# Performance work log

Hardware: AMD Instinct MI355X
Metric: run time of the kernel (lower is better)

## Reference

```python
import jax, jax.numpy as jnp
import numpy as np

N, E, F, H, ED, C, G = 50000, 800000, 86, 128, 16, 18, 64
NEG_SLOPE = 0.2


def setup_inputs() -> dict:
    key = jax.random.key(0)
    ks = jax.random.split(key, 20)
    s = 0.1
    return {
        "x": jax.random.normal(ks[0], (N, F), jnp.float32),
        "edge_index": jax.random.randint(ks[1], (2, E), 0, N, jnp.int32),
        "edge_attr": jax.random.normal(ks[2], (E, ED), jnp.float32),
        "batch": jnp.sort(jax.random.randint(ks[3], (N,), 0, G, jnp.int32)),
        # conv1 params (GATConv, heads=1): lin, lin_edge (no bias), att vectors, bias
        "W1": jax.random.normal(ks[4], (F, H), jnp.float32) * s,
        "We1": jax.random.normal(ks[5], (ED, H), jnp.float32) * s,
        "as1": jax.random.normal(ks[6], (H,), jnp.float32) * s,
        "ad1": jax.random.normal(ks[7], (H,), jnp.float32) * s,
        "ae1": jax.random.normal(ks[8], (H,), jnp.float32) * s,
        "b1": jnp.zeros((H,), jnp.float32),
        # conv2 params
        "W2": jax.random.normal(ks[9], (H, H), jnp.float32) * s,
        "We2": jax.random.normal(ks[10], (ED, H), jnp.float32) * s,
        "as2": jax.random.normal(ks[11], (H,), jnp.float32) * s,
        "ad2": jax.random.normal(ks[12], (H,), jnp.float32) * s,
        "ae2": jax.random.normal(ks[13], (H,), jnp.float32) * s,
        "b2": jnp.zeros((H,), jnp.float32),
        # final classifier
        "Wl": jax.random.normal(ks[14], (H, C), jnp.float32) * s,
        "bl": jnp.zeros((C,), jnp.float32),
    }


def gat_conv(x, edge_attr, src, dst, W, We, a_src, a_dst, a_edge, bias):
    h = x @ W                                   # [N, H]
    e = edge_attr @ We                          # [E, H]
    # per-edge attention logits: a_src.h_j + a_dst.h_i + a_edge.e
    alpha = (h @ a_src)[src] + (h @ a_dst)[dst] + e @ a_edge   # [E]
    alpha = jax.nn.leaky_relu(alpha, NEG_SLOPE)
    # segment softmax over incoming edges of each destination node
    m = jax.ops.segment_max(alpha, dst, num_segments=N)
    ex = jnp.exp(alpha - m[dst])
    denom = jax.ops.segment_sum(ex, dst, num_segments=N)
    w = ex / jnp.maximum(denom[dst], 1e-16)     # [E]
    out = jax.ops.segment_sum(h[src] * w[:, None], dst, num_segments=N)
    return out + bias


def reference(x, edge_index, edge_attr, batch,
              W1, We1, as1, ad1, ae1, b1,
              W2, We2, as2, ad2, ae2, b2,
              Wl, bl):
    src, dst = edge_index[0], edge_index[1]
    h = jax.nn.relu(gat_conv(x, edge_attr, src, dst, W1, We1, as1, ad1, ae1, b1))
    h = jax.nn.relu(gat_conv(h, edge_attr, src, dst, W2, We2, as2, ad2, ae2, b2))
    pooled = jax.ops.segment_max(h, batch, num_segments=G)      # [G, H] global max pool
    pooled = jnp.where(jnp.isfinite(pooled), pooled, 0.0)       # guard empty graphs
    logits = pooled @ Wl + bl                                   # [G, C]
    return jax.nn.log_softmax(logits, axis=-1)
```

## Files before the change

### kernel.cpp

```cpp
#include <hip/hip_runtime.h>
#include <math.h>

#define N_NODES 50000
#define N_EDGES 800000
#define F_IN    86
#define H_DIM   128
#define ED_DIM  16
#define C_CLS   18
#define G_GRAPHS 64
#define NEG_SLOPE 0.2f
#define SCAN_BLOCKS ((N_NODES + 255) / 256)
#define EB_BLOCKS ((N_EDGES + 255) / 256)
#define GB_BLOCKS ((N_NODES + 63) / 64)
#define HB_BLOCKS 782
#define HB_THREADS (HB_BLOCKS * 256)

typedef _Float16 h2v   __attribute__((ext_vector_type(2)));
typedef _Float16 half8 __attribute__((ext_vector_type(8)));
typedef float    f4v   __attribute__((ext_vector_type(4)));
typedef unsigned long long ull;

__device__ __forceinline__ void atomicMaxFloat(float* addr, float val) {
    if (val >= 0.0f) atomicMax((int*)addr, __float_as_int(val));
    else             atomicMin((unsigned int*)addr, __float_as_uint(val));
}

__global__ void prep(int* __restrict__ cnt0, int* __restrict__ cnt1,
                     float* __restrict__ pooled,
                     const float* __restrict__ We1, const float* __restrict__ ae1,
                     const float* __restrict__ We2, const float* __restrict__ ae2,
                     float* __restrict__ ve1, float* __restrict__ ve2,
                     const float* __restrict__ W1, const float* __restrict__ W2,
                     _Float16* __restrict__ w1t, _Float16* __restrict__ w2t) {
    int b = blockIdx.x, t = threadIdx.x;
    if (b < SCAN_BLOCKS) {
        int i = b * 256 + t;
        if (i < N_NODES) { cnt0[i] = 0; cnt1[i] = 0; }
    } else if (b == SCAN_BLOCKS) {
        if (t < ED_DIM) {
            float s = 0.f;
            for (int h = 0; h < H_DIM; ++h) s += We1[t * H_DIM + h] * ae1[h];
            ve1[t] = s;
        } else if (t < 2 * ED_DIM) {
            int j = t - ED_DIM;
            float s = 0.f;
            for (int h = 0; h < H_DIM; ++h) s += We2[j * H_DIM + h] * ae2[h];
            ve2[j] = s;
        }
        for (int i = t; i < G_GRAPHS * H_DIM; i += 256) pooled[i] = 0.f;
    } else if (b == SCAN_BLOCKS + 1) {
        for (int i = t; i < H_DIM * 96; i += 256) {
            int n = i / 96, k = i - n * 96;
            w1t[i] = (k < F_IN) ? (_Float16)W1[k * H_DIM + n] : (_Float16)0.f;
        }
    } else {
        for (int i = t; i < H_DIM * H_DIM; i += 256) {
            int n = i >> 7, k = i & 127;
            w2t[i] = (_Float16)W2[k * H_DIM + n];
        }
    }
}

__global__ void scan1(const int* __restrict__ cnt0, const int* __restrict__ cnt1,
                      int* __restrict__ excl, int* __restrict__ bsum) {
    __shared__ int s[256];
    int tid = threadIdx.x;
    int i = blockIdx.x * 256 + tid;
    int v = (i < N_NODES) ? cnt0[i] + cnt1[i] : 0;
    s[tid] = v;
    __syncthreads();
    for (int o = 1; o < 256; o <<= 1) {
        int t = (tid >= o) ? s[tid - o] : 0;
        __syncthreads();
        s[tid] += t;
        __syncthreads();
    }
    if (i < N_NODES) excl[i] = s[tid] - v;
    if (tid == 255) bsum[blockIdx.x] = s[255];
}

__global__ void scan_scatter(const int* __restrict__ excl, const int* __restrict__ bsum,
                             int* __restrict__ row_ptr,
                             const int* __restrict__ src, const int* __restrict__ dst,
                             const unsigned short* __restrict__ rank,
                             const int* __restrict__ cnt0,
                             const float* __restrict__ ea,
                             const float* __restrict__ ve1, const float* __restrict__ ve2,
                             int2* __restrict__ perm) {
    __shared__ int s[256];
    int tid = threadIdx.x;
    int v = (tid < SCAN_BLOCKS) ? bsum[tid] : 0;
    s[tid] = v;
    __syncthreads();
    for (int o = 1; o < 256; o <<= 1) {
        int t = (tid >= o) ? s[tid - o] : 0;
        __syncthreads();
        s[tid] += t;
        __syncthreads();
    }
    int eb = s[tid] - v;
    __syncthreads();
    s[tid] = eb;
    __syncthreads();
    int e = blockIdx.x * 256 + tid;
    if (blockIdx.x < SCAN_BLOCKS) {
        if (e < N_NODES) row_ptr[e] = excl[e] + s[e >> 8];
        if (e == 0) row_ptr[N_NODES] = N_EDGES;
    }
    if (e < N_EDGES) {
        int d = dst[e];
        int base = excl[d] + s[d >> 8];
        int off = (e & 1) ? cnt0[d] : 0;
        int pos = base + off + rank[e];
        const float4* p = (const float4*)(ea + (size_t)e * ED_DIM);
        float4 v0 = p[0], v1 = p[1], v2 = p[2], v3 = p[3];
        float s1 = v0.x*ve1[0] + v0.y*ve1[1] + v0.z*ve1[2] + v0.w*ve1[3]
                 + v1.x*ve1[4] + v1.y*ve1[5] + v1.z*ve1[6] + v1.w*ve1[7]
                 + v2.x*ve1[8] + v2.y*ve1[9] + v2.z*ve1[10] + v2.w*ve1[11]
                 + v3.x*ve1[12] + v3.y*ve1[13] + v3.z*ve1[14] + v3.w*ve1[15];
        float s2 = v0.x*ve2[0] + v0.y*ve2[1] + v0.z*ve2[2] + v0.w*ve2[3]
                 + v1.x*ve2[4] + v1.y*ve2[5] + v1.z*ve2[6] + v1.w*ve2[7]
                 + v2.x*ve2[8] + v2.y*ve2[9] + v2.z*ve2[10] + v2.w*ve2[11]
                 + v3.x*ve2[12] + v3.y*ve2[13] + v3.z*ve2[14] + v3.w*ve2[15];
        h2v dv;
        dv.x = (_Float16)s1;
        dv.y = (_Float16)s2;
        perm[pos] = make_int2(src[e], (int)__builtin_bit_cast(unsigned int, dv));
    }
}

#define KP1 104
__global__ __launch_bounds__(256)
void gemm1_hist(const float* __restrict__ in, const _Float16* __restrict__ w1t,
                const float* __restrict__ a_s, const float* __restrict__ a_d,
                _Float16* __restrict__ hout, float* __restrict__ hs, float* __restrict__ hd,
                const int* __restrict__ dst, int* __restrict__ cnt0, int* __restrict__ cnt1,
                unsigned short* __restrict__ rank) {
    __shared__ __attribute__((aligned(16))) _Float16 Asm[64 * KP1];
    __shared__ float sdots[64][2][2];
    int tid = threadIdx.x;

    if (blockIdx.x >= GB_BLOCKS) {
        int tbase = (blockIdx.x - GB_BLOCKS) * 256 + tid;
        int* bank = (tbase & 1) ? cnt1 : cnt0;
#pragma unroll
        for (int u = 0; u < 4; ++u) {
            int e = tbase + u * HB_THREADS;
            if (e < N_EDGES) {
                int r = atomicAdd(&bank[dst[e]], 1);
                rank[e] = (unsigned short)r;
            }
        }
        return;
    }

    int n0 = blockIdx.x * 64;
    const float2* in2 = (const float2*)(in + (size_t)n0 * F_IN);
    for (int idx = tid; idx < 64 * (F_IN / 2); idx += 256) {
        int r = idx / (F_IN / 2), k2 = idx - r * (F_IN / 2);
        float2 v = (n0 + r < N_NODES) ? in2[idx] : make_float2(0.f, 0.f);
        Asm[r * KP1 + 2 * k2]     = (_Float16)v.x;
        Asm[r * KP1 + 2 * k2 + 1] = (_Float16)v.y;
    }
    for (int idx = tid; idx < 64 * (96 - F_IN); idx += 256) {
        int r = idx / (96 - F_IN), k = F_IN + idx - r * (96 - F_IN);
        Asm[r * KP1 + k] = (_Float16)0.f;
    }
    __syncthreads();

    int wave = tid >> 6, lane = tid & 63;
    int wm = (wave & 1) * 32, wn = (wave >> 1) * 64;
    int m16 = lane & 15, quad = lane >> 4;

    f4v acc[2][4];
#pragma unroll
    for (int t = 0; t < 2; ++t)
#pragma unroll
        for (int c = 0; c < 4; ++c) acc[t][c] = (f4v){0.f, 0.f, 0.f, 0.f};

#pragma unroll
    for (int kk = 0; kk < 96 / 32; ++kk) {
        int koff = kk * 32 + quad * 8;
        half8 a0 = *(const half8*)&Asm[(wm + m16) * KP1 + koff];
        half8 a1 = *(const half8*)&Asm[(wm + 16 + m16) * KP1 + koff];
#pragma unroll
        for (int c = 0; c < 4; ++c) {
            half8 b = *(const half8*)&w1t[(wn + c * 16 + m16) * 96 + koff];
            acc[0][c] = __builtin_amdgcn_mfma_f32_16x16x32_f16(a0, b, acc[0][c], 0, 0, 0);
            acc[1][c] = __builtin_amdgcn_mfma_f32_16x16x32_f16(a1, b, acc[1][c], 0, 0, 0);
        }
    }

    float asv[4], adv[4];
#pragma unroll
    for (int c = 0; c < 4; ++c) {
        asv[c] = a_s[wn + c * 16 + m16];
        adv[c] = a_d[wn + c * 16 + m16];
    }
#pragma unroll
    for (int t = 0; t < 2; ++t)
#pragma unroll
        for (int r = 0; r < 4; ++r) {
            float ps = 0.f, pd = 0.f;
#pragma unroll
            for (int c = 0; c < 4; ++c) {
                float v = acc[t][c][r];
                ps += v * asv[c];
                pd += v * adv[c];
            }
#pragma unroll
            for (int o = 1; o < 16; o <<= 1) {
                ps += __shfl_xor(ps, o);
                pd += __shfl_xor(pd, o);
            }
            if (m16 == 0) {
                int row = wm + t * 16 + quad * 4 + r;
                sdots[row][wn >> 6][0] = ps;
                sdots[row][wn >> 6][1] = pd;
            }
        }
#pragma unroll
    for (int t = 0; t < 2; ++t)
#pragma unroll
        for (int c = 0; c < 4; ++c)
#pragma unroll
            for (int r = 0; r < 4; ++r) {
                int row = n0 + wm + t * 16 + quad * 4 + r;
                if (row < N_NODES)
                    hout[(size_t)row * H_DIM + wn + c * 16 + m16] = (_Float16)acc[t][c][r];
            }
    __syncthreads();
    if (tid < 64) {
        int row = n0 + tid;
        if (row < N_NODES) {
            hs[row] = sdots[tid][0][0] + sdots[tid][1][0];
            hd[row] = sdots[tid][0][1] + sdots[tid][1][1];
        }
    }
}

#define KP2 136
__global__ __launch_bounds__(256)
void gemm2(const _Float16* __restrict__ in, const _Float16* __restrict__ w2t,
           const float* __restrict__ a_s, const float* __restrict__ a_d,
           _Float16* __restrict__ hout, float* __restrict__ hs, float* __restrict__ hd) {
    __shared__ __attribute__((aligned(16))) _Float16 Asm[64 * KP2];
    __shared__ float sdots[64][2][2];
    int tid = threadIdx.x;
    int n0 = blockIdx.x * 64;

    const half8* in8 = (const half8*)(in + (size_t)n0 * H_DIM);
    for (int idx = tid; idx < 64 * 16; idx += 256) {
        int r = idx >> 4, k8 = idx & 15;
        half8 v = (n0 + r < N_NODES) ? in8[idx]
                                     : (half8){0, 0, 0, 0, 0, 0, 0, 0};
        *(half8*)&Asm[r * KP2 + k8 * 8] = v;
    }
    __syncthreads();

    int wave = tid >> 6, lane = tid & 63;
    int wm = (wave & 1) * 32, wn = (wave >> 1) * 64;
    int m16 = lane & 15, quad = lane >> 4;

    f4v acc[2][4];
#pragma unroll
    for (int t = 0; t < 2; ++t)
#pragma unroll
        for (int c = 0; c < 4; ++c) acc[t][c] = (f4v){0.f, 0.f, 0.f, 0.f};

#pragma unroll
    for (int kk = 0; kk < 128 / 32; ++kk) {
        int koff = kk * 32 + quad * 8;
        half8 a0 = *(const half8*)&Asm[(wm + m16) * KP2 + koff];
        half8 a1 = *(const half8*)&Asm[(wm + 16 + m16) * KP2 + koff];
#pragma unroll
        for (int c = 0; c < 4; ++c) {
            half8 b = *(const half8*)&w2t[(wn + c * 16 + m16) * H_DIM + koff];
            acc[0][c] = __builtin_amdgcn_mfma_f32_16x16x32_f16(a0, b, acc[0][c], 0, 0, 0);
            acc[1][c] = __builtin_amdgcn_mfma_f32_16x16x32_f16(a1, b, acc[1][c], 0, 0, 0);
        }
    }

    float asv[4], adv[4];
#pragma unroll
    for (int c = 0; c < 4; ++c) {
        asv[c] = a_s[wn + c * 16 + m16];
        adv[c] = a_d[wn + c * 16 + m16];
    }
#pragma unroll
    for (int t = 0; t < 2; ++t)
#pragma unroll
        for (int r = 0; r < 4; ++r) {
            float ps = 0.f, pd = 0.f;
#pragma unroll
            for (int c = 0; c < 4; ++c) {
                float v = acc[t][c][r];
                ps += v * asv[c];
                pd += v * adv[c];
            }
#pragma unroll
            for (int o = 1; o < 16; o <<= 1) {
                ps += __shfl_xor(ps, o);
                pd += __shfl_xor(pd, o);
            }
            if (m16 == 0) {
                int row = wm + t * 16 + quad * 4 + r;
                sdots[row][wn >> 6][0] = ps;
                sdots[row][wn >> 6][1] = pd;
            }
        }
#pragma unroll
    for (int t = 0; t < 2; ++t)
#pragma unroll
        for (int c = 0; c < 4; ++c)
#pragma unroll
            for (int r = 0; r < 4; ++r) {
                int row = n0 + wm + t * 16 + quad * 4 + r;
                if (row < N_NODES)
                    hout[(size_t)row * H_DIM + wn + c * 16 + m16] = (_Float16)acc[t][c][r];
            }
    __syncthreads();
    if (tid < 64) {
        int row = n0 + tid;
        if (row < N_NODES) {
            hs[row] = sdots[tid][0][0] + sdots[tid][1][0];
            hd[row] = sdots[tid][0][1] + sdots[tid][1][1];
        }
    }
}

template<int DOT, bool POOL>
__global__ void gat_node(const int* __restrict__ row_ptr, const int2* __restrict__ perm,
                         const float* __restrict__ hs, const float* __restrict__ hd,
                         const _Float16* __restrict__ h, const float* __restrict__ bias,
                         _Float16* __restrict__ out,
                         const int* __restrict__ batch, float* __restrict__ pooled) {
    __shared__ float smax[H_DIM];
    __shared__ int sg[4];
    __shared__ __attribute__((aligned(16))) ull stage[4][64];
    int tid = threadIdx.x;
    if (POOL) {
        if (tid < H_DIM) smax[tid] = 0.f;
        __syncthreads();
    }
    int n = blockIdx.x * 4 + (tid >> 6);
    int lane = tid & 63;
    int q = lane >> 4, m = lane & 15;
    int r0 = row_ptr[n], r1 = row_ptr[n + 1];
    float hdn = hd[n];
    const char* hb = (const char*)h;
    unsigned mo = (unsigned)(m * 16);
    ull* st = stage[tid >> 6];

    float acc[8];
#pragma unroll
    for (int k = 0; k < 8; ++k) acc[k] = 0.f;
    float denl = 0.f;

    for (int c = r0; c < r1; c += 64) {
        int i = c + lane;
        float w = 0.f;
        int so = 0;
        if (i < r1) {
            int2 p = perm[i];
            so = p.x * (H_DIM * 2);
            h2v dv = __builtin_bit_cast(h2v, p.y);
            float dotv = (DOT == 1) ? (float)dv.x : (float)dv.y;
            float t = hs[p.x] + hdn + dotv;
            t = (t > 0.f) ? t : NEG_SLOPE * t;
            w = __expf(t);
        }
        denl += w;
        st[lane] = (ull)(unsigned)so | ((ull)__float_as_uint(w) << 32);
        int lim = r1 - c; if (lim > 64) lim = 64;
        int njj = (lim + 7) >> 3;
        int jj = 0;
        for (; jj + 2 <= njj; jj += 2) {
            int b8 = jj << 3;
            ull p1 = st[b8 + q];
            ull p2 = st[b8 + q + 4];
            ull p3 = st[b8 + q + 8];
            ull p4 = st[b8 + q + 12];
            float w1 = __uint_as_float((unsigned)(p1 >> 32));
            float w2 = __uint_as_float((unsigned)(p2 >> 32));
            float w3 = __uint_as_float((unsigned)(p3 >> 32));
            float w4 = __uint_as_float((unsigned)(p4 >> 32));
            half8 v1 = *(const half8*)(hb + ((unsigned)p1 + mo));
            half8 v2 = *(const half8*)(hb + ((unsigned)p2 + mo));
            half8 v3 = *(const half8*)(hb + ((unsigned)p3 + mo));
            half8 v4 = *(const half8*)(hb + ((unsigned)p4 + mo));
#pragma unroll
            for (int k = 0; k < 8; ++k) acc[k] += w1 * (float)v1[k];
#pragma unroll
            for (int k = 0; k < 8; ++k) acc[k] += w2 * (float)v2[k];
#pragma unroll
            for (int k = 0; k < 8; ++k) acc[k] += w3 * (float)v3[k];
#pragma unroll
            for (int k = 0; k < 8; ++k) acc[k] += w4 * (float)v4[k];
        }
        if (jj < njj) {
            int b8 = jj << 3;
            ull p1 = st[b8 + q];
            ull p2 = st[b8 + q + 4];
            float w1 = __uint_as_float((unsigned)(p1 >> 32));
            float w2 = __uint_as_float((unsigned)(p2 >> 32));
            half8 v1 = *(const half8*)(hb + ((unsigned)p1 + mo));
            half8 v2 = *(const half8*)(hb + ((unsigned)p2 + mo));
#pragma unroll
            for (int k = 0; k < 8; ++k) acc[k] += w1 * (float)v1[k];
#pragma unroll
            for (int k = 0; k < 8; ++k) acc[k] += w2 * (float)v2[k];
        }
    }
#pragma unroll
    for (int k = 0; k < 8; ++k) {
        acc[k] += __shfl_xor(acc[k], 16);
        acc[k] += __shfl_xor(acc[k], 32);
    }
    float den = denl;
#pragma unroll
    for (int o = 32; o > 0; o >>= 1) den += __shfl_xor(den, o);
    float inv = 1.f / fmaxf(den, 1e-16f);

    float rv[8];
    if (q == 0) {
        float4 b0 = ((const float4*)bias)[2 * m];
        float4 b1 = ((const float4*)bias)[2 * m + 1];
        rv[0] = fmaxf(acc[0] * inv + b0.x, 0.f);
        rv[1] = fmaxf(acc[1] * inv + b0.y, 0.f);
        rv[2] = fmaxf(acc[2] * inv + b0.z, 0.f);
        rv[3] = fmaxf(acc[3] * inv + b0.w, 0.f);
        rv[4] = fmaxf(acc[4] * inv + b1.x, 0.f);
        rv[5] = fmaxf(acc[5] * inv + b1.y, 0.f);
        rv[6] = fmaxf(acc[6] * inv + b1.z, 0.f);
        rv[7] = fmaxf(acc[7] * inv + b1.w, 0.f);
    }

    if (!POOL) {
        if (q == 0) {
            half8 ov;
#pragma unroll
            for (int k = 0; k < 8; ++k) ov[k] = (_Float16)rv[k];
            *(half8*)&out[(size_t)n * H_DIM + m * 8] = ov;
        }
    } else {
        int g = batch[n];
        if (lane == 0) sg[tid >> 6] = g;
        if (q == 0) {
#pragma unroll
            for (int k = 0; k < 8; ++k)
                atomicMax((int*)&smax[m * 8 + k], __float_as_int(rv[k]));
        }
        __syncthreads();
        if (sg[0] == sg[3]) {
            if (tid < H_DIM)
                atomicMaxFloat(&pooled[sg[0] * H_DIM + tid], smax[tid]);
        } else {
            if (q == 0) {
#pragma unroll
                for (int k = 0; k < 8; ++k)
                    atomicMaxFloat(&pooled[g * H_DIM + m * 8 + k], rv[k]);
            }
        }
    }
}

__global__ void final_logits(const float* __restrict__ pooled, const float* __restrict__ Wl,
                             const float* __restrict__ bl, float* __restrict__ outp) {
    int g = threadIdx.x;
    if (g >= G_GRAPHS) return;
    float lg[C_CLS];
#pragma unroll
    for (int c = 0; c < C_CLS; ++c) lg[c] = bl[c];
    for (int k = 0; k < H_DIM; ++k) {
        float v = pooled[g * H_DIM + k];
#pragma unroll
        for (int c = 0; c < C_CLS; ++c) lg[c] += v * Wl[k * C_CLS + c];
    }
    float mx = lg[0];
#pragma unroll
    for (int c = 1; c < C_CLS; ++c) mx = fmaxf(mx, lg[c]);
    float se = 0.f;
#pragma unroll
    for (int c = 0; c < C_CLS; ++c) se += expf(lg[c] - mx);
    float lse = logf(se);
#pragma unroll
    for (int c = 0; c < C_CLS; ++c) outp[g * C_CLS + c] = lg[c] - mx - lse;
}

extern "C" void kernel_launch(void* const* d_in, const int* in_sizes, int n_in,
                              void* d_out, int out_size, void* d_ws, size_t ws_size,
                              hipStream_t stream) {
    const float* x     = (const float*)d_in[0];
    const int*   eidx  = (const int*)d_in[1];
    const float* ea    = (const float*)d_in[2];
    const int*   batch = (const int*)d_in[3];
    const float* W1  = (const float*)d_in[4];
    const float* We1 = (const float*)d_in[5];
    const float* as1 = (const float*)d_in[6];
    const float* ad1 = (const float*)d_in[7];
    const float* ae1 = (const float*)d_in[8];
    const float* b1  = (const float*)d_in[9];
    const float* W2  = (const float*)d_in[10];
    const float* We2 = (const float*)d_in[11];
    const float* as2 = (const float*)d_in[12];
    const float* ad2 = (const float*)d_in[13];
    const float* ae2 = (const float*)d_in[14];
    const float* b2  = (const float*)d_in[15];
    const float* Wl  = (const float*)d_in[16];
    const float* bl  = (const float*)d_in[17];
    float* outp = (float*)d_out;

    const int* src = eidx;
    const int* dst = eidx + N_EDGES;

    char* wsb = (char*)d_ws;
    size_t off = 0;
    auto alloc = [&](size_t bytes) { char* p = wsb + off; off += (bytes + 255) & ~(size_t)255; return p; };
    _Float16* h    = (_Float16*)alloc((size_t)N_NODES * H_DIM * 2);
    _Float16* A2   = (_Float16*)alloc((size_t)N_NODES * H_DIM * 2);
    int2*  perm    = (int2*)alloc((size_t)N_EDGES * 8);
    unsigned short* rank = (unsigned short*)alloc((size_t)N_EDGES * 2);
    float* hs      = (float*)alloc(N_NODES * 4);
    float* hd      = (float*)alloc(N_NODES * 4);
    int*   row_ptr = (int*)alloc((N_NODES + 1) * 4);
    int*   cnt0    = (int*)alloc(N_NODES * 4);
    int*   cnt1    = (int*)alloc(N_NODES * 4);
    int*   excl    = (int*)alloc(N_NODES * 4);
    int*   bsum    = (int*)alloc(SCAN_BLOCKS * 4);
    float* pooled  = (float*)alloc(G_GRAPHS * H_DIM * 4);
    float* ve1     = (float*)alloc(16 * 4);
    float* ve2     = (float*)alloc(16 * 4);
    _Float16* w1t  = (_Float16*)alloc(H_DIM * 96 * 2);
    _Float16* w2t  = (_Float16*)alloc(H_DIM * H_DIM * 2);

    const int NB4 = (N_NODES + 3) / 4;

    prep<<<SCAN_BLOCKS + 3, 256, 0, stream>>>(cnt0, cnt1, pooled, We1, ae1, We2, ae2,
                                              ve1, ve2, W1, W2, w1t, w2t);
    gemm1_hist<<<GB_BLOCKS + HB_BLOCKS, 256, 0, stream>>>(x, w1t, as1, ad1, h, hs, hd,
                                                          dst, cnt0, cnt1, rank);
    scan1<<<SCAN_BLOCKS, 256, 0, stream>>>(cnt0, cnt1, excl, bsum);
    scan_scatter<<<EB_BLOCKS, 256, 0, stream>>>(excl, bsum, row_ptr, src, dst,
                                                rank, cnt0, ea, ve1, ve2, perm);

    gat_node<1, false><<<NB4, 256, 0, stream>>>(row_ptr, perm, hs, hd, h, b1, A2,
                                                batch, pooled);

    gemm2<<<GB_BLOCKS, 256, 0, stream>>>(A2, w2t, as2, ad2, h, hs, hd);
    gat_node<2, true><<<NB4, 256, 0, stream>>>(row_ptr, perm, hs, hd, h, b2, nullptr,
                                               batch, pooled);

    final_logits<<<1, 64, 0, stream>>>(pooled, Wl, bl, outp);
}
```

Measured before the change: 310.8 us.

## Move edge-attr dot products into histogram blocks and widen counter banks to four

After: 301.4 us. -3.0%, faster.

```diff
diff --git a/kernel.cpp b/kernel.cpp
--- a/kernel.cpp
+++ b/kernel.cpp
@@ -25,8 +25,7 @@
     else             atomicMin((unsigned int*)addr, __float_as_uint(val));
 }
 
-__global__ void prep(int* __restrict__ cnt0, int* __restrict__ cnt1,
-                     float* __restrict__ pooled,
+__global__ void prep(int4* __restrict__ cnt4, float* __restrict__ pooled,
                      const float* __restrict__ We1, const float* __restrict__ ae1,
                      const float* __restrict__ We2, const float* __restrict__ ae2,
                      float* __restrict__ ve1, float* __restrict__ ve2,
@@ -35,7 +34,7 @@
     int b = blockIdx.x, t = threadIdx.x;
     if (b < SCAN_BLOCKS) {
         int i = b * 256 + t;
-        if (i < N_NODES) { cnt0[i] = 0; cnt1[i] = 0; }
+        if (i < N_NODES) cnt4[i] = make_int4(0, 0, 0, 0);
     } else if (b == SCAN_BLOCKS) {
         if (t < ED_DIM) {
             float s = 0.f;
@@ -61,12 +60,16 @@
     }
 }
 
-__global__ void scan1(const int* __restrict__ cnt0, const int* __restrict__ cnt1,
-                      int* __restrict__ excl, int* __restrict__ bsum) {
+__global__ void scan1(const int4* __restrict__ cnt4, int* __restrict__ excl,
+                      int* __restrict__ bsum) {
     __shared__ int s[256];
     int tid = threadIdx.x;
     int i = blockIdx.x * 256 + tid;
-    int v = (i < N_NODES) ? cnt0[i] + cnt1[i] : 0;
+    int v = 0;
+    if (i < N_NODES) {
+        int4 c = cnt4[i];
+        v = c.x + c.y + c.z + c.w;
+    }
     s[tid] = v;
     __syncthreads();
     for (int o = 1; o < 256; o <<= 1) {
@@ -83,9 +86,8 @@
                              int* __restrict__ row_ptr,
                              const int* __restrict__ src, const int* __restrict__ dst,
                              const unsigned short* __restrict__ rank,
-                             const int* __restrict__ cnt0,
-                             const float* __restrict__ ea,
-                             const float* __restrict__ ve1, const float* __restrict__ ve2,
+                             const int4* __restrict__ cnt4,
+                             const unsigned int* __restrict__ dotp,
                              int2* __restrict__ perm) {
     __shared__ int s[256];
     int tid = threadIdx.x;
@@ -109,23 +111,11 @@
     }
     if (e < N_EDGES) {
         int d = dst[e];
-        int base = excl[d] + s[d >> 8];
-        int off = (e & 1) ? cnt0[d] : 0;
-        int pos = base + off + rank[e];
-        const float4* p = (const float4*)(ea + (size_t)e * ED_DIM);
-        float4 v0 = p[0], v1 = p[1], v2 = p[2], v3 = p[3];
-        float s1 = v0.x*ve1[0] + v0.y*ve1[1] + v0.z*ve1[2] + v0.w*ve1[3]
-                 + v1.x*ve1[4] + v1.y*ve1[5] + v1.z*ve1[6] + v1.w*ve1[7]
-                 + v2.x*ve1[8] + v2.y*ve1[9] + v2.z*ve1[10] + v2.w*ve1[11]
-                 + v3.x*ve1[12] + v3.y*ve1[13] + v3.z*ve1[14] + v3.w*ve1[15];
-        float s2 = v0.x*ve2[0] + v0.y*ve2[1] + v0.z*ve2[2] + v0.w*ve2[3]
-                 + v1.x*ve2[4] + v1.y*ve2[5] + v1.z*ve2[6] + v1.w*ve2[7]
-                 + v2.x*ve2[8] + v2.y*ve2[9] + v2.z*ve2[10] + v2.w*ve2[11]
-                 + v3.x*ve2[12] + v3.y*ve2[13] + v3.z*ve2[14] + v3.w*ve2[15];
-        h2v dv;
-        dv.x = (_Float16)s1;
-        dv.y = (_Float16)s2;
-        perm[pos] = make_int2(src[e], (int)__builtin_bit_cast(unsigned int, dv));
+        int4 c = cnt4[d];
+        int bank = e & 3;
+        int off = (bank > 0 ? c.x : 0) + (bank > 1 ? c.y : 0) + (bank > 2 ? c.z : 0);
+        int pos = excl[d] + s[d >> 8] + off + rank[e];
+        perm[pos] = make_int2(src[e], (int)dotp[e]);
     }
 }
 
@@ -134,21 +124,37 @@
 void gemm1_hist(const float* __restrict__ in, const _Float16* __restrict__ w1t,
                 const float* __restrict__ a_s, const float* __restrict__ a_d,
                 _Float16* __restrict__ hout, float* __restrict__ hs, float* __restrict__ hd,
-                const int* __restrict__ dst, int* __restrict__ cnt0, int* __restrict__ cnt1,
-                unsigned short* __restrict__ rank) {
+                const int* __restrict__ dst, int* __restrict__ cnt,
+                unsigned short* __restrict__ rank, const float* __restrict__ ea,
+                const float* __restrict__ ve1, const float* __restrict__ ve2,
+                unsigned int* __restrict__ dotp) {
     __shared__ __attribute__((aligned(16))) _Float16 Asm[64 * KP1];
     __shared__ float sdots[64][2][2];
     int tid = threadIdx.x;
 
     if (blockIdx.x >= GB_BLOCKS) {
         int tbase = (blockIdx.x - GB_BLOCKS) * 256 + tid;
-        int* bank = (tbase & 1) ? cnt1 : cnt0;
+        int bank = tbase & 3;
 #pragma unroll
         for (int u = 0; u < 4; ++u) {
             int e = tbase + u * HB_THREADS;
             if (e < N_EDGES) {
-                int r = atomicAdd(&bank[dst[e]], 1);
+                int r = atomicAdd(&cnt[dst[e] * 4 + bank], 1);
                 rank[e] = (unsigned short)r;
+                const float4* p = (const float4*)(ea + (size_t)e * ED_DIM);
+                float4 v0 = p[0], v1 = p[1], v2 = p[2], v3 = p[3];
+                float s1 = v0.x*ve1[0] + v0.y*ve1[1] + v0.z*ve1[2] + v0.w*ve1[3]
+                         + v1.x*ve1[4] + v1.y*ve1[5] + v1.z*ve1[6] + v1.w*ve1[7]
+                         + v2.x*ve1[8] + v2.y*ve1[9] + v2.z*ve1[10] + v2.w*ve1[11]
+                         + v3.x*ve1[12] + v3.y*ve1[13] + v3.z*ve1[14] + v3.w*ve1[15];
+                float s2 = v0.x*ve2[0] + v0.y*ve2[1] + v0.z*ve2[2] + v0.w*ve2[3]
+                         + v1.x*ve2[4] + v1.y*ve2[5] + v1.z*ve2[6] + v1.w*ve2[7]
+                         + v2.x*ve2[8] + v2.y*ve2[9] + v2.z*ve2[10] + v2.w*ve2[11]
+                         + v3.x*ve2[12] + v3.y*ve2[13] + v3.z*ve2[14] + v3.w*ve2[15];
+                h2v dv;
+                dv.x = (_Float16)s1;
+                dv.y = (_Float16)s2;
+                dotp[e] = __builtin_bit_cast(unsigned int, dv);
             }
         }
         return;
@@ -521,11 +527,11 @@
     _Float16* A2   = (_Float16*)alloc((size_t)N_NODES * H_DIM * 2);
     int2*  perm    = (int2*)alloc((size_t)N_EDGES * 8);
     unsigned short* rank = (unsigned short*)alloc((size_t)N_EDGES * 2);
+    unsigned int* dotp = (unsigned int*)alloc((size_t)N_EDGES * 4);
     float* hs      = (float*)alloc(N_NODES * 4);
     float* hd      = (float*)alloc(N_NODES * 4);
     int*   row_ptr = (int*)alloc((N_NODES + 1) * 4);
-    int*   cnt0    = (int*)alloc(N_NODES * 4);
-    int*   cnt1    = (int*)alloc(N_NODES * 4);
+    int4*  cnt4    = (int4*)alloc((size_t)N_NODES * 16);
     int*   excl    = (int*)alloc(N_NODES * 4);
     int*   bsum    = (int*)alloc(SCAN_BLOCKS * 4);
     float* pooled  = (float*)alloc(G_GRAPHS * H_DIM * 4);
@@ -536,13 +542,14 @@
 
     const int NB4 = (N_NODES + 3) / 4;
 
-    prep<<<SCAN_BLOCKS + 3, 256, 0, stream>>>(cnt0, cnt1, pooled, We1, ae1, We2, ae2,
+    prep<<<SCAN_BLOCKS + 3, 256, 0, stream>>>(cnt4, pooled, We1, ae1, We2, ae2,
                                               ve1, ve2, W1, W2, w1t, w2t);
     gemm1_hist<<<GB_BLOCKS + HB_BLOCKS, 256, 0, stream>>>(x, w1t, as1, ad1, h, hs, hd,
-                                                          dst, cnt0, cnt1, rank);
-    scan1<<<SCAN_BLOCKS, 256, 0, stream>>>(cnt0, cnt1, excl, bsum);
+                                                          dst, (int*)cnt4, rank, ea,
+                                                          ve1, ve2, dotp);
+    scan1<<<SCAN_BLOCKS, 256, 0, stream>>>(cnt4, excl, bsum);
     scan_scatter<<<EB_BLOCKS, 256, 0, stream>>>(excl, bsum, row_ptr, src, dst,
-                                                rank, cnt0, ea, ve1, ve2, perm);
+                                                rank, cnt4, dotp, perm);
 
     gat_node<1, false><<<NB4, 256, 0, stream>>>(row_ptr, perm, hs, hd, h, b1, A2,
                                                 batch, pooled);
```
